# Kernel optimization log

Measured on AMD Instinct MI355X. Metric: run time of the kernel, lower is better.

## Reference

```python
import jax, jax.numpy as jnp
import numpy as np

N_HEADS, D_MODEL, DK, DV = 16, 1024, 64, 64
B, S = 4, 2048


def setup_inputs() -> dict:
    key = jax.random.key(0)
    ks = jax.random.split(key, 7)
    scale = 1.0 / np.sqrt(D_MODEL)
    return {
        "Q": jax.random.normal(ks[0], (B, S, D_MODEL), dtype=jnp.float32),
        "K": jax.random.normal(ks[1], (B, S, D_MODEL), dtype=jnp.float32),
        "V": jax.random.normal(ks[2], (B, S, D_MODEL), dtype=jnp.float32),
        # Linear weights stored as [in, out] so y = x @ W (equivalent to torch x @ W.T)
        "w_q": jax.random.normal(ks[3], (D_MODEL, N_HEADS * DK), dtype=jnp.float32) * scale,
        "w_k": jax.random.normal(ks[4], (D_MODEL, N_HEADS * DK), dtype=jnp.float32) * scale,
        "w_v": jax.random.normal(ks[5], (D_MODEL, N_HEADS * DV), dtype=jnp.float32) * scale,
        "w_o": jax.random.normal(ks[6], (N_HEADS * DV, D_MODEL), dtype=jnp.float32) * scale,
    }


def reference(Q, K, V, w_q, w_k, w_v, w_o):
    b, s, _ = Q.shape
    # projections -> [B, H, S, d]
    q = (Q @ w_q).reshape(b, s, N_HEADS, DK).transpose(0, 2, 1, 3)
    k = (K @ w_k).reshape(b, s, N_HEADS, DK).transpose(0, 2, 1, 3)
    v = (V @ w_v).reshape(b, s, N_HEADS, DV).transpose(0, 2, 1, 3)
    # scaled dot-product attention, full [B,H,S,S] scores (matches source)
    scores = jnp.einsum("bhqd,bhkd->bhqk", q, k) / jnp.sqrt(jnp.float32(DK))
    attn = jax.nn.softmax(scores, axis=-1)
    x = jnp.einsum("bhqk,bhkd->bhqd", attn, v)
    x = x.transpose(0, 2, 1, 3).reshape(b, s, N_HEADS * DV)
    return x @ w_o
```

## Files before the change

kernel.cpp:

```cpp
#include <hip/hip_runtime.h>
#include <stdint.h>

#define B_   4
#define S_   2048
#define H_   16
#define D_   64
#define DM_  1024
#define NTOK (B_ * S_)

typedef __attribute__((ext_vector_type(8))) short short8;
typedef __attribute__((ext_vector_type(4))) float floatx4;

__device__ inline unsigned short f2bf(float f) {
  unsigned int u = __float_as_uint(f);
  u += 0x7FFFu + ((u >> 16) & 1u);
  return (unsigned short)(u >> 16);
}

__device__ inline floatx4 mfma_bf16(short8 a, short8 b, floatx4 c) {
  return __builtin_amdgcn_mfma_f32_16x16x32_bf16(a, b, c, 0, 0, 0);
}

__device__ inline unsigned int pack_bf2(float lo, float hi) {
  return __builtin_amdgcn_perm(__float_as_uint(hi), __float_as_uint(lo), 0x07060302u);
}

__device__ inline unsigned int cvt_pk_bf16(float lo, float hi) {
  unsigned int r;
  asm("v_cvt_pk_bf16_f32 %0, %1, %2" : "=v"(r) : "v"(lo), "v"(hi));
  return r;
}

__device__ inline void gload_lds16(const unsigned short* g, unsigned short* l) {
  __builtin_amdgcn_global_load_lds(
      (const __attribute__((address_space(1))) unsigned int*)g,
      (__attribute__((address_space(3))) unsigned int*)l, 16, 0, 0);
}

__global__ __launch_bounds__(256) void wt_kernel(const float* __restrict__ w0,
                                                 const float* __restrict__ w1,
                                                 const float* __restrict__ w2,
                                                 const float* __restrict__ w3,
                                                 unsigned short* __restrict__ o0,
                                                 unsigned short* __restrict__ o1,
                                                 unsigned short* __restrict__ o2,
                                                 unsigned short* __restrict__ o3) {
  __shared__ unsigned short T[64 * 68];
  const float* w = blockIdx.z == 0 ? w0 : blockIdx.z == 1 ? w1 : blockIdx.z == 2 ? w2 : w3;
  unsigned short* o = blockIdx.z == 0 ? o0 : blockIdx.z == 1 ? o1 : blockIdx.z == 2 ? o2 : o3;
  const int tid = threadIdx.x;
  const int R0 = blockIdx.y * 64;
  const int C0 = blockIdx.x * 64;
  for (int it = 0; it < 16; it++) {
    int lr = it * 4 + (tid >> 6), lc = tid & 63;
    T[lc * 68 + lr] = f2bf(w[(size_t)(R0 + lr) * 1024 + C0 + lc]);
  }
  __syncthreads();
  for (int it = 0; it < 2; it++) {
    int orow = it * 32 + (tid >> 3), oc = (tid & 7) * 8;
    union { ushort4 h[2]; short8 v8; } u;
    u.h[0] = *(const ushort4*)(T + orow * 68 + oc);
    u.h[1] = *(const ushort4*)(T + orow * 68 + oc + 4);
    *(short8*)(o + (size_t)(C0 + orow) * 1024 + R0 + oc) = u.v8;
  }
}


__global__ __launch_bounds__(256) void proj_kernel(
    const float* __restrict__ Qf, const float* __restrict__ Kf,
    const float* __restrict__ Vf,
    const unsigned short* __restrict__ wqT, const unsigned short* __restrict__ wkT,
    const unsigned short* __restrict__ wvT,
    unsigned short* __restrict__ qP, unsigned short* __restrict__ kP,
    unsigned short* __restrict__ vTg, float sc) {
  constexpr int K = 1024;
  __shared__ __align__(16) float          As[128 * 32];
  __shared__ __align__(16) unsigned short Bs[128 * 32];

  const int z = blockIdx.z;
  const float* A           = z == 0 ? Qf  : z == 1 ? Kf  : Vf;
  const unsigned short* BT = z == 0 ? wqT : z == 1 ? wkT : wvT;
  unsigned short* Cout     = z == 0 ? qP  : z == 1 ? kP  : vTg;
  const float scale        = z == 0 ? sc : 1.0f;
  const int mode           = (z == 2) ? 2 : 0;

  const int tid  = threadIdx.x;
  const int wave = tid >> 6, lane = tid & 63;
  const int quad = lane >> 4, l16 = lane & 15;
  const int wm = wave >> 1, wn = wave & 1;
  const int mb = blockIdx.x * 8 + (blockIdx.y >> 3);
  const int nb = blockIdx.y & 7;
  const int m0 = mb * 128, n0 = nb * 128;

  floatx4 acc[4][4] = {};

  for (int k0 = 0; k0 < K; k0 += 32) {
    for (int p = 0; p < 4; p++) {
      int si = p * 256 + tid;
      int r = si >> 3;
      int gc = (si & 7) ^ (r & 7);
      gload_lds16((const unsigned short*)(A + (size_t)(m0 + r) * K + k0 + gc * 4),
                  (unsigned short*)As + (size_t)(p * 256 + wave * 64) * 8);
    }
    for (int p = 0; p < 2; p++) {
      int si = p * 256 + tid;
      int R = si >> 3;
      int gc = (si & 7) ^ (R & 7);
      gload_lds16(BT + (size_t)(n0 + R * 2 + (gc >> 2)) * K + k0 + (gc & 3) * 8,
                  Bs + (size_t)(p * 256 + wave * 64) * 8);
    }
    __syncthreads();

    short8 af[4], bfr[4];
    for (int f = 0; f < 4; f++) {
      int ra = wm * 64 + f * 16 + l16;
      int swa = ra & 7;
      float4 a0 = *(const float4*)(As + ra * 32 + ((2 * quad) ^ swa) * 4);
      float4 a1 = *(const float4*)(As + ra * 32 + ((2 * quad + 1) ^ swa) * 4);
      union { unsigned int u[4]; short8 s8; } pk;
      pk.u[0] = cvt_pk_bf16(a0.x, a0.y);
      pk.u[1] = cvt_pk_bf16(a0.z, a0.w);
      pk.u[2] = cvt_pk_bf16(a1.x, a1.y);
      pk.u[3] = cvt_pk_bf16(a1.z, a1.w);
      af[f] = pk.s8;
      int rb = wn * 64 + f * 16 + l16;
      int slb = (((rb & 1) * 4 + quad) ^ ((rb >> 1) & 7));
      bfr[f] = *(const short8*)(Bs + (rb >> 1) * 64 + slb * 8);
    }
    for (int fm = 0; fm < 4; fm++)
      for (int fn = 0; fn < 4; fn++)
        acc[fm][fn] = mfma_bf16(af[fm], bfr[fn], acc[fm][fn]);
    __syncthreads();
  }

  for (int fm = 0; fm < 4; fm++)
    for (int fn = 0; fn < 4; fn++)
      for (int r = 0; r < 4; r++) {
        int gm = m0 + wm * 64 + fm * 16 + quad * 4 + r;
        int gn = n0 + wn * 64 + fn * 16 + l16;
        float val = acc[fm][fn][r] * scale;
        int b = gm >> 11, s = gm & 2047;
        int h = gn >> 6,  d = gn & 63;
        if (mode == 0) {
          Cout[((size_t)((b * H_ + h) * S_ + s) << 6) + d] = f2bf(val);
        } else {
          int p = ((s & 63) >> 4) + (s & 15) * 4;
          Cout[(((size_t)(b * H_ + h) * 64 + d) << 11) + (s & ~63) + p] = f2bf(val);
        }
      }
}

template <int MODE>
__global__ __launch_bounds__(256) void gemm_bt_kernel(const unsigned short* __restrict__ A,
                                                      const unsigned short* __restrict__ BT,
                                                      void* __restrict__ Cout,
                                                      float scale) {
  constexpr int K = 1024;
  __shared__ __align__(16) unsigned short As[128 * 32];
  __shared__ __align__(16) unsigned short Bs[128 * 32];

  const int tid  = threadIdx.x;
  const int wave = tid >> 6, lane = tid & 63;
  const int quad = lane >> 4, l16 = lane & 15;
  const int wm = wave >> 1, wn = wave & 1;
  const int mb = blockIdx.x * 8 + (blockIdx.y >> 3);
  const int nb = blockIdx.y & 7;
  const int m0 = mb * 128, n0 = nb * 128;

  floatx4 acc[4][4] = {};

  for (int k0 = 0; k0 < K; k0 += 32) {
    for (int p = 0; p < 2; p++) {
      int si = p * 256 + tid;
      int R = si >> 3;
      int gc = (si & 7) ^ (R & 7);
      int r = R * 2 + (gc >> 2), c = gc & 3;
      gload_lds16(A  + (size_t)(m0 + r) * K + k0 + c * 8,
                  As + (size_t)(p * 256 + wave * 64) * 8);
      gload_lds16(BT + (size_t)(n0 + r) * K + k0 + c * 8,
                  Bs + (size_t)(p * 256 + wave * 64) * 8);
    }
    __syncthreads();

    short8 af[4], bfr[4];
    for (int f = 0; f < 4; f++) {
      int ra = wm * 64 + f * 16 + l16;
      int sla = (((ra & 1) * 4 + quad) ^ ((ra >> 1) & 7));
      af[f] = *(const short8*)(As + (ra >> 1) * 64 + sla * 8);
      int rb = wn * 64 + f * 16 + l16;
      int slb = (((rb & 1) * 4 + quad) ^ ((rb >> 1) & 7));
      bfr[f] = *(const short8*)(Bs + (rb >> 1) * 64 + slb * 8);
    }
    for (int fm = 0; fm < 4; fm++)
      for (int fn = 0; fn < 4; fn++)
        acc[fm][fn] = mfma_bf16(af[fm], bfr[fn], acc[fm][fn]);
    __syncthreads();
  }

  for (int fm = 0; fm < 4; fm++)
    for (int fn = 0; fn < 4; fn++)
      for (int r = 0; r < 4; r++) {
        int gm = m0 + wm * 64 + fm * 16 + quad * 4 + r;
        int gn = n0 + wn * 64 + fn * 16 + l16;
        float val = acc[fm][fn][r] * scale;
        if (MODE == 0) {
          int b = gm >> 11, s = gm & 2047;
          int h = gn >> 6,  d = gn & 63;
          ((unsigned short*)Cout)[((size_t)((b * H_ + h) * S_ + s) << 6) + d] = f2bf(val);
        } else if (MODE == 1) {
          ((float*)Cout)[((size_t)gm << 10) + gn] = val;
        } else {
          int b = gm >> 11, s = gm & 2047;
          int h = gn >> 6,  d = gn & 63;
          int p = ((s & 63) >> 4) + (s & 15) * 4;
          ((unsigned short*)Cout)[(((size_t)(b * H_ + h) * 64 + d) << 11) + (s & ~63) + p] = f2bf(val);
        }
      }
}

__global__ __launch_bounds__(512, 4) void attn_kernel(const unsigned short* __restrict__ q,
                                                      const unsigned short* __restrict__ k,
                                                      const unsigned short* __restrict__ vT,
                                                      unsigned short* __restrict__ X) {
  __shared__ unsigned short Ks[2][64 * 64];
  __shared__ unsigned short Vt[2][64 * 64];
  __shared__ unsigned short Ps[8][16 * 72];

  const int tid  = threadIdx.x;
  const int wave = tid >> 6, lane = tid & 63;
  const int quad = lane >> 4, l16 = lane & 15;
  const int bh = blockIdx.x * 8 + (blockIdx.y >> 3);
  const int q0 = (blockIdx.y & 7) * 256;

  const unsigned short* qh = q  + (size_t)bh * S_ * 64;
  const unsigned short* kh = k  + (size_t)bh * S_ * 64;
  const unsigned short* vh = vT + (size_t)bh * 64 * S_;

  const int sr  = tid >> 3;
  const int sgc = (tid & 7) ^ (sr & 7);

  short8 qf[2][2];
  for (int qt = 0; qt < 2; qt++) {
    int row = q0 + wave * 32 + qt * 16 + l16;
    for (int kk = 0; kk < 2; kk++)
      qf[qt][kk] = *(const short8*)(qh + (size_t)row * 64 + kk * 32 + quad * 8);
  }

  short8 onesb = {};
  if (l16 == 0)
    for (int e = 0; e < 8; e++) onesb[e] = (short)0x3F80;

  const floatx4 fz = {};
  floatx4 O[2][4] = {};
  floatx4 lacc[2] = {};

  gload_lds16(kh + (size_t)sr * 64 + sgc * 8,       Ks[0] + (size_t)(wave * 64) * 8);
  gload_lds16(vh + (size_t)sr * S_ + 0 + sgc * 8,   Vt[0] + (size_t)(wave * 64) * 8);

  int cur = 0;
  for (int j0 = 0; j0 < S_; j0 += 64) {
    __syncthreads();

    if (j0 + 64 < S_) {
      int nxt = cur ^ 1;
      gload_lds16(kh + (size_t)(j0 + 64 + sr) * 64 + sgc * 8,
                  Ks[nxt] + (size_t)(wave * 64) * 8);
      gload_lds16(vh + (size_t)sr * S_ + (j0 + 64) + sgc * 8,
                  Vt[nxt] + (size_t)(wave * 64) * 8);
    }

    short8 kf[4][2];
    for (int jf = 0; jf < 4; jf++)
      for (int kk = 0; kk < 2; kk++) {
        int sl = (kk * 4 + quad) ^ (l16 & 7);
        kf[jf][kk] = *(const short8*)(Ks[cur] + (jf * 16 + l16) * 64 + sl * 8);
      }

    unsigned short* pw = Ps[wave];
    short8 pa[2][2];
    for (int qt = 0; qt < 2; qt++) {
      floatx4 s[4];
      for (int jf = 0; jf < 4; jf++) {
        s[jf] = mfma_bf16(qf[qt][0], kf[jf][0], fz);
        s[jf] = mfma_bf16(qf[qt][1], kf[jf][1], s[jf]);
      }
      for (int r = 0; r < 4; r++) {
        float e0 = __builtin_amdgcn_exp2f(s[0][r]);
        float e1 = __builtin_amdgcn_exp2f(s[1][r]);
        float e2 = __builtin_amdgcn_exp2f(s[2][r]);
        float e3 = __builtin_amdgcn_exp2f(s[3][r]);
        uint2 pk;
        pk.x = pack_bf2(e0, e1);
        pk.y = pack_bf2(e2, e3);
        *(uint2*)(pw + (quad * 4 + r) * 72 + l16 * 4) = pk;
      }
      pa[qt][0] = *(const short8*)(pw + l16 * 72 + quad * 8);
      pa[qt][1] = *(const short8*)(pw + l16 * 72 + 32 + quad * 8);
      lacc[qt] = mfma_bf16(pa[qt][0], onesb, lacc[qt]);
      lacc[qt] = mfma_bf16(pa[qt][1], onesb, lacc[qt]);
    }

    for (int df = 0; df < 4; df++) {
      int sl0 = quad ^ (l16 & 7);
      int sl1 = (4 + quad) ^ (l16 & 7);
      short8 v0 = *(const short8*)(Vt[cur] + (df * 16 + l16) * 64 + sl0 * 8);
      short8 v1 = *(const short8*)(Vt[cur] + (df * 16 + l16) * 64 + sl1 * 8);
      for (int qt = 0; qt < 2; qt++) {
        O[qt][df] = mfma_bf16(pa[qt][0], v0, O[qt][df]);
        O[qt][df] = mfma_bf16(pa[qt][1], v1, O[qt][df]);
      }
    }
    cur ^= 1;
  }

  const int b = bh >> 4, h = bh & 15;
  for (int qt = 0; qt < 2; qt++)
    for (int r = 0; r < 4; r++) {
      float lsum = __shfl(lacc[qt][r], (lane & 48));
      float inv = 1.0f / lsum;
      int row = q0 + wave * 32 + qt * 16 + quad * 4 + r;
      unsigned short* dst = X + ((size_t)(b * S_ + row) << 10) + h * 64;
      for (int df = 0; df < 4; df++)
        dst[df * 16 + l16] = f2bf(O[qt][df][r] * inv);
    }
}

extern "C" void kernel_launch(void* const* d_in, const int* in_sizes, int n_in,
                              void* d_out, int out_size, void* d_ws, size_t ws_size,
                              hipStream_t stream) {
  const float* Q  = (const float*)d_in[0];
  const float* K  = (const float*)d_in[1];
  const float* V  = (const float*)d_in[2];
  const float* wq = (const float*)d_in[3];
  const float* wk = (const float*)d_in[4];
  const float* wv = (const float*)d_in[5];
  const float* wo = (const float*)d_in[6];

  char* ws = (char*)d_ws;
  unsigned short* buf0 = (unsigned short*)ws;
  unsigned short* wqT  = (unsigned short*)(ws + (size_t)(16 << 20));
  unsigned short* wkT  = (unsigned short*)(ws + (size_t)(18 << 20));
  unsigned short* wvT  = (unsigned short*)(ws + (size_t)(20 << 20));
  unsigned short* woT  = (unsigned short*)(ws + (size_t)(22 << 20));
  unsigned short* qP   = (unsigned short*)(ws + (size_t)(24 << 20));
  unsigned short* kP   = (unsigned short*)(ws + (size_t)(40 << 20));
  unsigned short* vTg  = (unsigned short*)(ws + (size_t)(56 << 20));

  const float SC = 0.18033688011112043f;

  wt_kernel<<<dim3(16, 16, 4), dim3(256), 0, stream>>>(wq, wk, wv, wo, wqT, wkT, wvT, woT);

  proj_kernel<<<dim3(8, 64, 3), dim3(256), 0, stream>>>(Q, K, V, wqT, wkT, wvT,
                                                        qP, kP, vTg, SC);

  attn_kernel<<<dim3(8, 64), dim3(512), 0, stream>>>(qP, kP, vTg, buf0);

  gemm_bt_kernel<1><<<dim3(8, 64), dim3(256), 0, stream>>>(buf0, woT, (float*)d_out, 1.0f);
}
```

Baseline: 358.1 us.

## Double-buffer LDS tiles in projection and output GEMM kernels

Both the fused QKV projection kernel and the generic GEMM kernel now keep two shared-memory buffers for the A and B tiles. The loads for the next K-slice are issued right after the barrier, so they run while the MFMA work on the current slice proceeds, and the second barrier per iteration is dropped. This is meant to hide global-to-LDS latency in the GEMM stages. It doubles LDS use per block, which may lower occupancy, and the compiler may still insert conservative vmcnt waits that serialize the async loads.

```diff
diff --git a/kernel.cpp b/kernel.cpp
--- a/kernel.cpp
+++ b/kernel.cpp
@@ -74,8 +74,8 @@
     unsigned short* __restrict__ qP, unsigned short* __restrict__ kP,
     unsigned short* __restrict__ vTg, float sc) {
   constexpr int K = 1024;
-  __shared__ __align__(16) float          As[128 * 32];
-  __shared__ __align__(16) unsigned short Bs[128 * 32];
+  __shared__ __align__(16) float          As[2][128 * 32];
+  __shared__ __align__(16) unsigned short Bs[2][128 * 32];
 
   const int z = blockIdx.z;
   const float* A           = z == 0 ? Qf  : z == 1 ? Kf  : Vf;
@@ -92,31 +92,43 @@
   const int nb = blockIdx.y & 7;
   const int m0 = mb * 128, n0 = nb * 128;
 
+  const int srA  = tid >> 3;
+  const int sgcA = (tid & 7) ^ (srA & 7);
+  const int sRB  = tid >> 3;
+  const int sgcB = (tid & 7) ^ (sRB & 7);
+
   floatx4 acc[4][4] = {};
 
+#define STAGE_PROJ(k0, buf)                                                        \
+  do {                                                                             \
+    for (int p = 0; p < 4; p++) {                                                  \
+      int r = (p * 256 + tid) >> 3;                                                \
+      int gc = ((p * 256 + tid) & 7) ^ (r & 7);                                    \
+      gload_lds16((const unsigned short*)(A + (size_t)(m0 + r) * K + (k0) + gc * 4), \
+                  (unsigned short*)As[buf] + (size_t)(p * 256 + wave * 64) * 8);   \
+    }                                                                              \
+    for (int p = 0; p < 2; p++) {                                                  \
+      int R = (p * 256 + tid) >> 3;                                                \
+      int gc = ((p * 256 + tid) & 7) ^ (R & 7);                                    \
+      gload_lds16(BT + (size_t)(n0 + R * 2 + (gc >> 2)) * K + (k0) + (gc & 3) * 8, \
+                  Bs[buf] + (size_t)(p * 256 + wave * 64) * 8);                    \
+    }                                                                              \
+  } while (0)
+
+  STAGE_PROJ(0, 0);
+
+  int cur = 0;
   for (int k0 = 0; k0 < K; k0 += 32) {
-    for (int p = 0; p < 4; p++) {
-      int si = p * 256 + tid;
-      int r = si >> 3;
-      int gc = (si & 7) ^ (r & 7);
-      gload_lds16((const unsigned short*)(A + (size_t)(m0 + r) * K + k0 + gc * 4),
-                  (unsigned short*)As + (size_t)(p * 256 + wave * 64) * 8);
-    }
-    for (int p = 0; p < 2; p++) {
-      int si = p * 256 + tid;
-      int R = si >> 3;
-      int gc = (si & 7) ^ (R & 7);
-      gload_lds16(BT + (size_t)(n0 + R * 2 + (gc >> 2)) * K + k0 + (gc & 3) * 8,
-                  Bs + (size_t)(p * 256 + wave * 64) * 8);
-    }
     __syncthreads();
+
+    if (k0 + 32 < K) STAGE_PROJ(k0 + 32, cur ^ 1);
 
     short8 af[4], bfr[4];
     for (int f = 0; f < 4; f++) {
       int ra = wm * 64 + f * 16 + l16;
       int swa = ra & 7;
-      float4 a0 = *(const float4*)(As + ra * 32 + ((2 * quad) ^ swa) * 4);
-      float4 a1 = *(const float4*)(As + ra * 32 + ((2 * quad + 1) ^ swa) * 4);
+      float4 a0 = *(const float4*)(As[cur] + ra * 32 + ((2 * quad) ^ swa) * 4);
+      float4 a1 = *(const float4*)(As[cur] + ra * 32 + ((2 * quad + 1) ^ swa) * 4);
       union { unsigned int u[4]; short8 s8; } pk;
       pk.u[0] = cvt_pk_bf16(a0.x, a0.y);
       pk.u[1] = cvt_pk_bf16(a0.z, a0.w);
@@ -125,13 +137,14 @@
       af[f] = pk.s8;
       int rb = wn * 64 + f * 16 + l16;
       int slb = (((rb & 1) * 4 + quad) ^ ((rb >> 1) & 7));
-      bfr[f] = *(const short8*)(Bs + (rb >> 1) * 64 + slb * 8);
+      bfr[f] = *(const short8*)(Bs[cur] + (rb >> 1) * 64 + slb * 8);
     }
     for (int fm = 0; fm < 4; fm++)
       for (int fn = 0; fn < 4; fn++)
         acc[fm][fn] = mfma_bf16(af[fm], bfr[fn], acc[fm][fn]);
-    __syncthreads();
-  }
+    cur ^= 1;
+  }
+#undef STAGE_PROJ
 
   for (int fm = 0; fm < 4; fm++)
     for (int fn = 0; fn < 4; fn++)
@@ -156,8 +169,8 @@
                                                       void* __restrict__ Cout,
                                                       float scale) {
   constexpr int K = 1024;
-  __shared__ __align__(16) unsigned short As[128 * 32];
-  __shared__ __align__(16) unsigned short Bs[128 * 32];
+  __shared__ __align__(16) unsigned short As[2][128 * 32];
+  __shared__ __align__(16) unsigned short Bs[2][128 * 32];
 
   const int tid  = threadIdx.x;
   const int wave = tid >> 6, lane = tid & 63;
@@ -169,33 +182,43 @@
 
   floatx4 acc[4][4] = {};
 
+#define STAGE_GEMM(k0, buf)                                                     \
+  do {                                                                          \
+    for (int p = 0; p < 2; p++) {                                               \
+      int si = p * 256 + tid;                                                   \
+      int R = si >> 3;                                                          \
+      int gc = (si & 7) ^ (R & 7);                                              \
+      int r = R * 2 + (gc >> 2), c = gc & 3;                                    \
+      gload_lds16(A  + (size_t)(m0 + r) * K + (k0) + c * 8,                     \
+                  As[buf] + (size_t)(p * 256 + wave * 64) * 8);                 \
+      gload_lds16(BT + (size_t)(n0 + r) * K + (k0) + c * 8,                     \
+                  Bs[buf] + (size_t)(p * 256 + wave * 64) * 8);                 \
+    }                                                                           \
+  } while (0)
+
+  STAGE_GEMM(0, 0);
+
+  int cur = 0;
   for (int k0 = 0; k0 < K; k0 += 32) {
-    for (int p = 0; p < 2; p++) {
-      int si = p * 256 + tid;
-      int R = si >> 3;
-      int gc = (si & 7) ^ (R & 7);
-      int r = R * 2 + (gc >> 2), c = gc & 3;
-      gload_lds16(A  + (size_t)(m0 + r) * K + k0 + c * 8,
-                  As + (size_t)(p * 256 + wave * 64) * 8);
-      gload_lds16(BT + (size_t)(n0 + r) * K + k0 + c * 8,
-                  Bs + (size_t)(p * 256 + wave * 64) * 8);
-    }
     __syncthreads();
+
+    if (k0 + 32 < K) STAGE_GEMM(k0 + 32, cur ^ 1);
 
     short8 af[4], bfr[4];
     for (int f = 0; f < 4; f++) {
       int ra = wm * 64 + f * 16 + l16;
       int sla = (((ra & 1) * 4 + quad) ^ ((ra >> 1) & 7));
-      af[f] = *(const short8*)(As + (ra >> 1) * 64 + sla * 8);
+      af[f] = *(const short8*)(As[cur] + (ra >> 1) * 64 + sla * 8);
       int rb = wn * 64 + f * 16 + l16;
       int slb = (((rb & 1) * 4 + quad) ^ ((rb >> 1) & 7));
-      bfr[f] = *(const short8*)(Bs + (rb >> 1) * 64 + slb * 8);
+      bfr[f] = *(const short8*)(Bs[cur] + (rb >> 1) * 64 + slb * 8);
     }
     for (int fm = 0; fm < 4; fm++)
       for (int fn = 0; fn < 4; fn++)
         acc[fm][fn] = mfma_bf16(af[fm], bfr[fn], acc[fm][fn]);
-    __syncthreads();
-  }
+    cur ^= 1;
+  }
+#undef STAGE_GEMM
 
   for (int fm = 0; fm < 4; fm++)
     for (int fn = 0; fn < 4; fn++)
```

Result: no change. 352.1 us (-1.7%).
